# Kernel optimization log

Measured on AMD Instinct MI355X. Metric: run time of the kernel, lower is better.

## Reference

```python
import jax, jax.numpy as jnp
import numpy as np

B, S, K, N, GROUP = 4, 8, 4096, 11008, 128
NUM_GROUPS = K // GROUP  # 32


def setup_inputs() -> dict:
    key = jax.random.key(0)
    k1, k2, k3 = jax.random.split(key, 3)
    x = jax.random.normal(k1, (B, S, K), dtype=jnp.float16)
    # packed int4 weights: each byte holds two nibbles (low nibble = even k, high = odd k)
    weight_packed = jax.random.randint(k2, (N, K // 2), 0, 256, dtype=jnp.int32)
    # scales: abs(randn)*0.1 in fp16, as in the torch module
    scales = (jnp.abs(jax.random.normal(k3, (N, NUM_GROUPS), dtype=jnp.float16)) * jnp.float16(0.1))
    return {"x": x, "weight_packed": weight_packed, "scales": scales}


def _dequant(weight_packed, scales, Kd):
    # unpack: low nibble -> even index k, high nibble -> odd index k+1
    n = weight_packed.shape[0]
    low = weight_packed & 0xF
    high = (weight_packed >> 4) & 0xF
    w = jnp.stack([low, high], axis=-1).reshape(n, Kd)  # [N, K] int in [0,16)
    g = Kd // scales.shape[1]
    # group-wise dequant: scale * (w - 8), scale applied in fp32 (matches fp32-accum kernel)
    wq = (w.astype(jnp.float32) - 8.0).reshape(n, scales.shape[1], g)
    wdeq = wq * scales.astype(jnp.float32)[:, :, None]
    return wdeq.reshape(n, Kd)  # [N, K] fp32


def reference(x, weight_packed, scales):
    b, s, kd = x.shape
    wdeq = _dequant(weight_packed, scales, kd)           # [N, K]
    x2 = x.reshape(-1, kd).astype(jnp.float32)           # [M, K], fp32 accumulation
    out = jnp.einsum('mk,nk->mn', x2, wdeq)              # [M, N]
    return out.astype(jnp.float16).reshape(b, s, -1)
```

## Files before the change

kernel.cpp:

```cpp
#include <hip/hip_runtime.h>

#define M 32
#define N 11008
#define K 4096
#define NGROUPS 32
#define BN 64
#define KSPLIT 16
#define KRANGE (K / KSPLIT)
#define MN (M * N)

typedef _Float16 half8 __attribute__((ext_vector_type(8)));
typedef _Float16 half4 __attribute__((ext_vector_type(4)));
typedef float floatx4 __attribute__((ext_vector_type(4)));

#define WPAIR 260
#define XPAIR 520

__device__ inline void gll16(const void* g, void* l) {
    __builtin_amdgcn_global_load_lds(
        (const __attribute__((address_space(1))) unsigned int*)g,
        (__attribute__((address_space(3))) unsigned int*)l, 16, 0, 0);
}

__global__ __launch_bounds__(512) void xcvt_kernel(
    const float* __restrict__ x, _Float16* __restrict__ xf)
{
    int i = (blockIdx.x * 512 + threadIdx.x) * 4;
    float4 v = *(const float4*)(x + i);
    half4 h;
    h[0] = (_Float16)v.x; h[1] = (_Float16)v.y;
    h[2] = (_Float16)v.z; h[3] = (_Float16)v.w;
    *(half4*)(xf + i) = h;
}

__global__ __launch_bounds__(256) void int4_gemm_kernel(
    const _Float16* __restrict__ xf,
    const int* __restrict__ wp,
    const float* __restrict__ scales,
    float* __restrict__ part)
{
    __shared__ int wsh[32 * WPAIR];
    __shared__ _Float16 xs[16 * XPAIR];

    const int t    = threadIdx.x;
    const int lane = t & 63;
    const int w    = t >> 6;
    const int n0   = blockIdx.x * BN;
    const int ks   = blockIdx.y;
    const int row  = lane & 15;
    const int quad = lane >> 4;

    const int nw = n0 + w * 16 + row;
    const float s0 = scales[nw * NGROUPS + ks * 2];
    const float s1 = scales[nw * NGROUPS + ks * 2 + 1];

    #pragma unroll
    for (int i = 0; i < 8; ++i) {
        int p = w * 8 + i;
        int r = 2 * p + (lane >> 5);
        const int* g = wp + (long)(n0 + r) * (K / 2) + ks * (KRANGE / 2) + (lane & 31) * 4;
        gll16(g, &wsh[p * WPAIR]);
    }
    #pragma unroll
    for (int i = 0; i < 4; ++i) {
        int p = w * 4 + i;
        int m = 2 * p + (lane >> 5);
        const _Float16* g = xf + m * K + ks * KRANGE + (lane & 31) * 8;
        gll16(g, &xs[p * XPAIR]);
    }
    __syncthreads();

    const half8 c1032 = (half8)(_Float16)1032.0f;
    floatx4 acc0 = {0.f, 0.f, 0.f, 0.f};
    floatx4 acc1 = {0.f, 0.f, 0.f, 0.f};

    const int wr    = w * 16 + row;
    const int wbase = (wr >> 1) * WPAIR + (wr & 1) * 128 + quad * 4;
    const int xbase = (row >> 1) * XPAIR + (row & 1) * 256 + quad * 8;

    #pragma unroll
    for (int g = 0; g < 2; ++g) {
        floatx4 t0 = {0.f, 0.f, 0.f, 0.f};
        floatx4 t1 = {0.f, 0.f, 0.f, 0.f};
        #pragma unroll
        for (int kk = 0; kk < 4; ++kk) {
            const int kq = g * 4 + kk;
            int4 wv = *(const int4*)&wsh[wbase + kq * 16];
            uint4 uw;
            {
                unsigned int b;
                b = (unsigned int)wv.x; uw.x = ((b | (b << 12)) & 0x000F000Fu) | 0x64006400u;
                b = (unsigned int)wv.y; uw.y = ((b | (b << 12)) & 0x000F000Fu) | 0x64006400u;
                b = (unsigned int)wv.z; uw.z = ((b | (b << 12)) & 0x000F000Fu) | 0x64006400u;
                b = (unsigned int)wv.w; uw.w = ((b | (b << 12)) & 0x000F000Fu) | 0x64006400u;
            }
            half8 bfrag = __builtin_bit_cast(half8, uw) - c1032;
            half8 a0 = *(const half8*)&xs[xbase + kq * 32];
            half8 a1 = *(const half8*)&xs[xbase + 8 * XPAIR + kq * 32];
            t0 = __builtin_amdgcn_mfma_f32_16x16x32_f16(a0, bfrag, t0, 0, 0, 0);
            t1 = __builtin_amdgcn_mfma_f32_16x16x32_f16(a1, bfrag, t1, 0, 0, 0);
        }
        const float s = g ? s1 : s0;
        #pragma unroll
        for (int r = 0; r < 4; ++r) {
            acc0[r] += s * t0[r];
            acc1[r] += s * t1[r];
        }
    }

    float* po = part + (long)ks * MN;
    #pragma unroll
    for (int r = 0; r < 4; ++r) {
        int mr = quad * 4 + r;
        po[mr * N + nw]        = acc0[r];
        po[(mr + 16) * N + nw] = acc1[r];
    }
}

__global__ __launch_bounds__(256) void reduce_kernel(
    const float* __restrict__ part, float* __restrict__ out)
{
    int o = blockIdx.x * 256 + threadIdx.x;
    float s = 0.f;
    #pragma unroll
    for (int j = 0; j < KSPLIT; ++j) s += part[(long)j * MN + o];
    out[o] = s;
}

extern "C" void kernel_launch(void* const* d_in, const int* in_sizes, int n_in,
                              void* d_out, int out_size, void* d_ws, size_t ws_size,
                              hipStream_t stream) {
    const float* x      = (const float*)d_in[0];
    const int* wp       = (const int*)d_in[1];
    const float* scales = (const float*)d_in[2];
    float* out          = (float*)d_out;

    _Float16* xf16 = (_Float16*)d_ws;
    float* part    = (float*)((char*)d_ws + (size_t)M * K * 2);

    xcvt_kernel<<<dim3((M * K) / (512 * 4)), 512, 0, stream>>>(x, xf16);
    int4_gemm_kernel<<<dim3(N / BN, KSPLIT), 256, 0, stream>>>(xf16, wp, scales, part);
    reduce_kernel<<<dim3(MN / 256), 256, 0, stream>>>(part, out);
}
```

Measured before the change: 145.7 us.

## Fuse fp32-to-fp16 activation conversion into GEMM and reorder grid dimensions

Drops the separate conversion kernel. Each GEMM block now loads fp32 activations directly, converts them to fp16 in registers and stores them to LDS, which removes one kernel launch and a round trip through global memory. The grid is also swapped so that consecutive blocks share an N tile across K splits, which may change cache locality for the weight and activation reads. In exchange, each block reads twice as many activation bytes and the async global-to-LDS load for x becomes a synchronous register path.

```diff
diff --git a/kernel.cpp b/kernel.cpp
--- a/kernel.cpp
+++ b/kernel.cpp
@@ -10,7 +10,6 @@
 #define MN (M * N)
 
 typedef _Float16 half8 __attribute__((ext_vector_type(8)));
-typedef _Float16 half4 __attribute__((ext_vector_type(4)));
 typedef float floatx4 __attribute__((ext_vector_type(4)));
 
 #define WPAIR 260
@@ -22,19 +21,8 @@
         (__attribute__((address_space(3))) unsigned int*)l, 16, 0, 0);
 }
 
-__global__ __launch_bounds__(512) void xcvt_kernel(
-    const float* __restrict__ x, _Float16* __restrict__ xf)
-{
-    int i = (blockIdx.x * 512 + threadIdx.x) * 4;
-    float4 v = *(const float4*)(x + i);
-    half4 h;
-    h[0] = (_Float16)v.x; h[1] = (_Float16)v.y;
-    h[2] = (_Float16)v.z; h[3] = (_Float16)v.w;
-    *(half4*)(xf + i) = h;
-}
-
 __global__ __launch_bounds__(256) void int4_gemm_kernel(
-    const _Float16* __restrict__ xf,
+    const float* __restrict__ x,
     const int* __restrict__ wp,
     const float* __restrict__ scales,
     float* __restrict__ part)
@@ -45,8 +33,8 @@
     const int t    = threadIdx.x;
     const int lane = t & 63;
     const int w    = t >> 6;
-    const int n0   = blockIdx.x * BN;
-    const int ks   = blockIdx.y;
+    const int ks   = blockIdx.x;
+    const int n0   = blockIdx.y * BN;
     const int row  = lane & 15;
     const int quad = lane >> 4;
 
@@ -65,8 +53,15 @@
     for (int i = 0; i < 4; ++i) {
         int p = w * 4 + i;
         int m = 2 * p + (lane >> 5);
-        const _Float16* g = xf + m * K + ks * KRANGE + (lane & 31) * 8;
-        gll16(g, &xs[p * XPAIR]);
+        const float* g = x + m * K + ks * KRANGE + (lane & 31) * 8;
+        float4 v0 = *(const float4*)g;
+        float4 v1 = *(const float4*)(g + 4);
+        half8 h;
+        h[0] = (_Float16)v0.x; h[1] = (_Float16)v0.y;
+        h[2] = (_Float16)v0.z; h[3] = (_Float16)v0.w;
+        h[4] = (_Float16)v1.x; h[5] = (_Float16)v1.y;
+        h[6] = (_Float16)v1.z; h[7] = (_Float16)v1.w;
+        *(half8*)&xs[p * XPAIR + (lane >> 5) * 256 + (lane & 31) * 8] = h;
     }
     __syncthreads();
 
@@ -134,11 +129,8 @@
     const int* wp       = (const int*)d_in[1];
     const float* scales = (const float*)d_in[2];
     float* out          = (float*)d_out;
+    float* part         = (float*)d_ws;
 
-    _Float16* xf16 = (_Float16*)d_ws;
-    float* part    = (float*)((char*)d_ws + (size_t)M * K * 2);
-
-    xcvt_kernel<<<dim3((M * K) / (512 * 4)), 512, 0, stream>>>(x, xf16);
-    int4_gemm_kernel<<<dim3(N / BN, KSPLIT), 256, 0, stream>>>(xf16, wp, scales, part);
+    int4_gemm_kernel<<<dim3(KSPLIT, N / BN), 256, 0, stream>>>(x, wp, scales, part);
     reduce_kernel<<<dim3(MN / 256), 256, 0, stream>>>(part, out);
 }
```

Result: no change. 146.2 us (+0.3%).

## Loop four N-tiles per block with double-buffered LDS weight staging and register-held activations

Applied to the files above, without the earlier changes.

Each block now covers 256 output columns as four 64-wide tiles. Weight loads go into per-wave double-buffered LDS via global_load_lds, with manual waitcnt so the next tile's load overlaps MFMA work on the current one. Activations move from LDS into registers and are loaded once per block, and the grid axes are swapped so K-split blocks with the same N are adjacent. This cuts the grid to a quarter of the blocks and hides load latency, at the cost of more registers, less parallelism, and hand-coded waitcnt encodings that are easy to get wrong.

```diff
diff --git a/kernel.cpp b/kernel.cpp
--- a/kernel.cpp
+++ b/kernel.cpp
@@ -4,9 +4,9 @@
 #define N 11008
 #define K 4096
 #define NGROUPS 32
-#define BN 64
 #define KSPLIT 16
 #define KRANGE (K / KSPLIT)
+#define NTILE 4
 #define MN (M * N)
 
 typedef _Float16 half8 __attribute__((ext_vector_type(8)));
@@ -14,7 +14,10 @@
 typedef float floatx4 __attribute__((ext_vector_type(4)));
 
 #define WPAIR 260
-#define XPAIR 520
+
+#define WAITVM8()   __builtin_amdgcn_s_waitcnt(0x0F78)
+#define WAITVM0()   __builtin_amdgcn_s_waitcnt(0x0F70)
+#define WAITLGKM0() __builtin_amdgcn_s_waitcnt(0xC07F)
 
 __device__ inline void gll16(const void* g, void* l) {
     __builtin_amdgcn_global_load_lds(
@@ -33,88 +36,106 @@
     *(half4*)(xf + i) = h;
 }
 
-__global__ __launch_bounds__(256) void int4_gemm_kernel(
+__global__ __launch_bounds__(256, 2) void int4_gemm_kernel(
     const _Float16* __restrict__ xf,
     const int* __restrict__ wp,
     const float* __restrict__ scales,
     float* __restrict__ part)
 {
-    __shared__ int wsh[32 * WPAIR];
-    __shared__ _Float16 xs[16 * XPAIR];
+    __shared__ int wsh[4 * 2 * 8 * WPAIR];
 
-    const int t    = threadIdx.x;
-    const int lane = t & 63;
-    const int w    = t >> 6;
-    const int n0   = blockIdx.x * BN;
-    const int ks   = blockIdx.y;
-    const int row  = lane & 15;
-    const int quad = lane >> 4;
+    const int t     = threadIdx.x;
+    const int lane  = t & 63;
+    const int w     = t >> 6;
+    const int ks    = blockIdx.x;
+    const int nbase = blockIdx.y * 256;
+    const int row   = lane & 15;
+    const int quad  = lane >> 4;
+    const int k0    = ks * KRANGE;
 
-    const int nw = n0 + w * 16 + row;
-    const float s0 = scales[nw * NGROUPS + ks * 2];
-    const float s1 = scales[nw * NGROUPS + ks * 2 + 1];
+    half8 af[8][2];
+    #pragma unroll
+    for (int kk = 0; kk < 8; ++kk)
+        #pragma unroll
+        for (int i = 0; i < 2; ++i)
+            af[kk][i] = *(const half8*)(xf + (i * 16 + row) * K + k0 + kk * 32 + quad * 8);
 
+    float sc[NTILE][2];
     #pragma unroll
-    for (int i = 0; i < 8; ++i) {
-        int p = w * 8 + i;
-        int r = 2 * p + (lane >> 5);
-        const int* g = wp + (long)(n0 + r) * (K / 2) + ks * (KRANGE / 2) + (lane & 31) * 4;
-        gll16(g, &wsh[p * WPAIR]);
+    for (int tt = 0; tt < NTILE; ++tt) {
+        int nw = nbase + tt * 64 + w * 16 + row;
+        sc[tt][0] = scales[nw * NGROUPS + ks * 2];
+        sc[tt][1] = scales[nw * NGROUPS + ks * 2 + 1];
     }
-    #pragma unroll
-    for (int i = 0; i < 4; ++i) {
-        int p = w * 4 + i;
-        int m = 2 * p + (lane >> 5);
-        const _Float16* g = xf + m * K + ks * KRANGE + (lane & 31) * 8;
-        gll16(g, &xs[p * XPAIR]);
-    }
-    __syncthreads();
+
+    auto stage = [&](int tt, int buf) {
+        const long rbase = nbase + tt * 64 + w * 16;
+        #pragma unroll
+        for (int p = 0; p < 8; ++p) {
+            const int* g = wp + (rbase + 2 * p + (lane >> 5)) * (long)(K / 2)
+                         + ks * (KRANGE / 2) + (lane & 31) * 4;
+            gll16(g, &wsh[((w * 2 + buf) * 8 + p) * WPAIR]);
+        }
+    };
 
     const half8 c1032 = (half8)(_Float16)1032.0f;
-    floatx4 acc0 = {0.f, 0.f, 0.f, 0.f};
-    floatx4 acc1 = {0.f, 0.f, 0.f, 0.f};
 
-    const int wr    = w * 16 + row;
-    const int wbase = (wr >> 1) * WPAIR + (wr & 1) * 128 + quad * 4;
-    const int xbase = (row >> 1) * XPAIR + (row & 1) * 256 + quad * 8;
-
-    #pragma unroll
-    for (int g = 0; g < 2; ++g) {
-        floatx4 t0 = {0.f, 0.f, 0.f, 0.f};
-        floatx4 t1 = {0.f, 0.f, 0.f, 0.f};
+    auto compute = [&](int tt, int buf) {
+        floatx4 acc0 = {0.f, 0.f, 0.f, 0.f};
+        floatx4 acc1 = {0.f, 0.f, 0.f, 0.f};
+        const int wb = (w * 2 + buf) * 8 * WPAIR + (row >> 1) * WPAIR
+                     + (row & 1) * 128 + quad * 4;
         #pragma unroll
-        for (int kk = 0; kk < 4; ++kk) {
-            const int kq = g * 4 + kk;
-            int4 wv = *(const int4*)&wsh[wbase + kq * 16];
-            uint4 uw;
-            {
-                unsigned int b;
-                b = (unsigned int)wv.x; uw.x = ((b | (b << 12)) & 0x000F000Fu) | 0x64006400u;
-                b = (unsigned int)wv.y; uw.y = ((b | (b << 12)) & 0x000F000Fu) | 0x64006400u;
-                b = (unsigned int)wv.z; uw.z = ((b | (b << 12)) & 0x000F000Fu) | 0x64006400u;
-                b = (unsigned int)wv.w; uw.w = ((b | (b << 12)) & 0x000F000Fu) | 0x64006400u;
+        for (int g = 0; g < 2; ++g) {
+            floatx4 t0 = {0.f, 0.f, 0.f, 0.f};
+            floatx4 t1 = {0.f, 0.f, 0.f, 0.f};
+            #pragma unroll
+            for (int k4 = 0; k4 < 4; ++k4) {
+                const int kq = g * 4 + k4;
+                int4 wv = *(const int4*)&wsh[wb + kq * 16];
+                uint4 uw;
+                {
+                    unsigned int b;
+                    b = (unsigned int)wv.x; uw.x = ((b | (b << 12)) & 0x000F000Fu) | 0x64006400u;
+                    b = (unsigned int)wv.y; uw.y = ((b | (b << 12)) & 0x000F000Fu) | 0x64006400u;
+                    b = (unsigned int)wv.z; uw.z = ((b | (b << 12)) & 0x000F000Fu) | 0x64006400u;
+                    b = (unsigned int)wv.w; uw.w = ((b | (b << 12)) & 0x000F000Fu) | 0x64006400u;
+                }
+                half8 bfrag = __builtin_bit_cast(half8, uw) - c1032;
+                t0 = __builtin_amdgcn_mfma_f32_16x16x32_f16(af[kq][0], bfrag, t0, 0, 0, 0);
+                t1 = __builtin_amdgcn_mfma_f32_16x16x32_f16(af[kq][1], bfrag, t1, 0, 0, 0);
             }
-            half8 bfrag = __builtin_bit_cast(half8, uw) - c1032;
-            half8 a0 = *(const half8*)&xs[xbase + kq * 32];
-            half8 a1 = *(const half8*)&xs[xbase + 8 * XPAIR + kq * 32];
-            t0 = __builtin_amdgcn_mfma_f32_16x16x32_f16(a0, bfrag, t0, 0, 0, 0);
-            t1 = __builtin_amdgcn_mfma_f32_16x16x32_f16(a1, bfrag, t1, 0, 0, 0);
+            const float s = sc[tt][g];
+            #pragma unroll
+            for (int r = 0; r < 4; ++r) {
+                acc0[r] += s * t0[r];
+                acc1[r] += s * t1[r];
+            }
         }
-        const float s = g ? s1 : s0;
+        float* po = part + (long)ks * MN;
+        const int nw = nbase + tt * 64 + w * 16 + row;
         #pragma unroll
         for (int r = 0; r < 4; ++r) {
-            acc0[r] += s * t0[r];
-            acc1[r] += s * t1[r];
+            int mr = quad * 4 + r;
+            po[mr * N + nw]        = acc0[r];
+            po[(mr + 16) * N + nw] = acc1[r];
         }
-    }
+    };
 
-    float* po = part + (long)ks * MN;
-    #pragma unroll
-    for (int r = 0; r < 4; ++r) {
-        int mr = quad * 4 + r;
-        po[mr * N + nw]        = acc0[r];
-        po[(mr + 16) * N + nw] = acc1[r];
-    }
+    stage(0, 0);
+    stage(1, 1);
+    WAITVM8();
+    compute(0, 0);
+    WAITLGKM0();
+    stage(2, 0);
+    WAITVM8();
+    compute(1, 1);
+    WAITLGKM0();
+    stage(3, 1);
+    WAITVM8();
+    compute(2, 0);
+    WAITVM0();
+    compute(3, 1);
 }
 
 __global__ __launch_bounds__(256) void reduce_kernel(
@@ -139,6 +160,6 @@
     float* part    = (float*)((char*)d_ws + (size_t)M * K * 2);
 
     xcvt_kernel<<<dim3((M * K) / (512 * 4)), 512, 0, stream>>>(x, xf16);
-    int4_gemm_kernel<<<dim3(N / BN, KSPLIT), 256, 0, stream>>>(xf16, wp, scales, part);
+    int4_gemm_kernel<<<dim3(KSPLIT, N / 256), 256, 0, stream>>>(xf16, wp, scales, part);
     reduce_kernel<<<dim3(MN / 256), 256, 0, stream>>>(part, out);
 }
```

After: 151.8 us. 4.2% more time.
